# Kernel tuning notes

Hardware: AMD Instinct MI355X
Metric: run time of the kernel (lower is better)

The kernel has to match this reference:

```python
import jax, jax.numpy as jnp
import numpy as np

MARGIN = 0.3
LAMBDA_TRIPLET = 1.0
LAMBDA_ID = 1.0
EPS = 1e-6  # torch pairwise_distance eps added to the difference elementwise


def setup_inputs() -> dict:
    key = jax.random.key(0)
    k1, k2 = jax.random.split(key)
    B, N, D = 64, 512, 512
    reid_features = jax.random.normal(k1, (B, N, D), dtype=jnp.float32)
    # ids in [-1, 32): -1 marks invalid detections, as in the torch module
    track_ids = jax.random.randint(k2, (B, N), -1, 32, dtype=jnp.int32)
    return {"reid_features": reid_features, "track_ids": track_ids}


def _tracking_loss(feats, ids, margin):
    B, N, D = feats.shape
    valid = ids >= 0                                   # (B, N)
    same = ids[:, :, None] == ids[:, None, :]          # (B, N, N)
    not_self = ~jnp.eye(N, dtype=bool)                 # (N, N)
    valid_j = valid[:, None, :]                        # candidates must be valid
    pos_mask = same & not_self & valid_j               # (B, N, N)
    neg_mask = (~same) & valid_j                       # (B, N, N)
    has_pos = pos_mask.any(-1)                         # (B, N)
    has_neg = neg_mask.any(-1)
    enough = valid.sum(-1) >= 2                        # (B,)
    anchor_ok = valid & has_pos & has_neg & enough[:, None]
    # torch.nonzero(mask)[0] == first True index -> argmax on bool
    pos_idx = jnp.argmax(pos_mask, axis=-1)            # (B, N)
    neg_idx = jnp.argmax(neg_mask, axis=-1)
    p = jnp.take_along_axis(feats, pos_idx[..., None], axis=1)  # (B, N, D)
    n = jnp.take_along_axis(feats, neg_idx[..., None], axis=1)
    d_ap = jnp.sqrt(jnp.sum((feats - p + EPS) ** 2, axis=-1))   # (B, N)
    d_an = jnp.sqrt(jnp.sum((feats - n + EPS) ** 2, axis=-1))
    per_anchor = jnp.maximum(d_ap - d_an + margin, 0.0)
    num_triplets = anchor_ok.sum()
    total = jnp.sum(per_anchor * anchor_ok.astype(feats.dtype))
    loss = jnp.where(num_triplets > 0,
                     total / jnp.maximum(num_triplets, 1).astype(feats.dtype),
                     jnp.zeros((), feats.dtype))
    return loss * LAMBDA_TRIPLET


def reference(reid_features, track_ids):
    loss_triplet = _tracking_loss(reid_features, track_ids, MARGIN)
    loss_id = jnp.zeros((), reid_features.dtype)
    tracking_loss = loss_triplet + loss_id
    return tracking_loss, loss_triplet, loss_id
```

## Files before the change

### kernel.cpp

```cpp
#include <hip/hip_runtime.h>

#define MARGIN 0.3f
#define EPS 1e-6f

constexpr int B = 64, N = 512, D = 512;
constexpr int NIDS = 32;
constexpr int BLOCKS = 512;
constexpr int THREADS = 512;
constexpr int WAVES = THREADS / 64;
constexpr int ANCH_PER_BLOCK = N / 8;
constexpr int ANCH_PER_WAVE = ANCH_PER_BLOCK / WAVES;

__global__ __launch_bounds__(THREADS) void tl_main(const float* __restrict__ feats,
                                                   const int* __restrict__ ids,
                                                   float* __restrict__ psum,
                                                   float* __restrict__ pcnt) {
    __shared__ int s_ids[N];
    __shared__ int s_first[NIDS], s_second[NIDS];
    __shared__ int s_j0, s_jdiff, s_vcnt;
    __shared__ float s_wsum[WAVES];
    __shared__ int s_wcnt[WAVES];

    const int t = threadIdx.x;
    const int b = blockIdx.x >> 3;
    const int seg = (blockIdx.x & 7) * ANCH_PER_BLOCK;
    const int* __restrict__ bid = ids + b * N;

    if (t < NIDS) { s_first[t] = N; s_second[t] = N; }
    if (t == 0) { s_j0 = N; s_jdiff = N; s_vcnt = 0; }
    __syncthreads();

    {
        const int v = bid[t];
        s_ids[t] = v;
        if (v >= 0) {
            atomicMin(&s_first[v], t);
            atomicMin(&s_j0, t);
            atomicAdd(&s_vcnt, 1);
        }
    }
    __syncthreads();
    const int id0 = (s_j0 < N) ? s_ids[s_j0] : -2;
    {
        const int v = s_ids[t];
        if (v >= 0) {
            if (s_first[v] != t) atomicMin(&s_second[v], t);
            if (v != id0) atomicMin(&s_jdiff, t);
        }
    }
    __syncthreads();

    const int lane = t & 63;
    const int wave = t >> 6;
    const float* __restrict__ bf = feats + (size_t)b * N * D;
    const int vcnt = s_vcnt;
    const int j0 = s_j0, jdiff = s_jdiff;

    float wsum = 0.0f;
    int wcnt = 0;

    #pragma unroll
    for (int k = 0; k < ANCH_PER_WAVE; ++k) {
        const int i = seg + wave * ANCH_PER_WAVE + k;
        const int v = s_ids[i];
        bool ok = false;
        int posj = 0, negj = 0;
        if (v >= 0 && vcnt >= 2) {
            posj = (s_first[v] != i) ? s_first[v] : s_second[v];
            negj = (id0 != v) ? j0 : jdiff;
            ok = (posj < N) && (negj < N);
        }
        if (ok) {
            const float4* fa = (const float4*)(bf + (size_t)i * D) + lane * 2;
            const float4* fp = (const float4*)(bf + (size_t)posj * D) + lane * 2;
            const float4* fn = (const float4*)(bf + (size_t)negj * D) + lane * 2;
            float sap = 0.0f, san = 0.0f;
            #pragma unroll
            for (int q = 0; q < 2; ++q) {
                const float4 a = fa[q];
                const float4 p = fp[q];
                const float4 n = fn[q];
                float d;
                d = a.x - p.x + EPS; sap += d * d;
                d = a.y - p.y + EPS; sap += d * d;
                d = a.z - p.z + EPS; sap += d * d;
                d = a.w - p.w + EPS; sap += d * d;
                d = a.x - n.x + EPS; san += d * d;
                d = a.y - n.y + EPS; san += d * d;
                d = a.z - n.z + EPS; san += d * d;
                d = a.w - n.w + EPS; san += d * d;
            }
            #pragma unroll
            for (int off = 32; off >= 1; off >>= 1) {
                sap += __shfl_xor(sap, off);
                san += __shfl_xor(san, off);
            }
            wsum += fmaxf(sqrtf(sap) - sqrtf(san) + MARGIN, 0.0f);
            ++wcnt;
        }
    }

    if (lane == 0) { s_wsum[wave] = wsum; s_wcnt[wave] = wcnt; }
    __syncthreads();
    if (t == 0) {
        float s = 0.0f; int c = 0;
        #pragma unroll
        for (int w = 0; w < WAVES; ++w) { s += s_wsum[w]; c += s_wcnt[w]; }
        psum[blockIdx.x] = s;
        pcnt[blockIdx.x] = (float)c;
    }
}

__global__ __launch_bounds__(256) void tl_finalize(const float* __restrict__ psum,
                                                   const float* __restrict__ pcnt,
                                                   float* __restrict__ out) {
    __shared__ float s_s[4], s_c[4];
    const int t = threadIdx.x;
    float s = 0.0f, c = 0.0f;
    for (int k = t; k < BLOCKS; k += 256) { s += psum[k]; c += pcnt[k]; }
    #pragma unroll
    for (int off = 32; off >= 1; off >>= 1) {
        s += __shfl_xor(s, off);
        c += __shfl_xor(c, off);
    }
    if ((t & 63) == 0) { s_s[t >> 6] = s; s_c[t >> 6] = c; }
    __syncthreads();
    if (t == 0) {
        const float S = s_s[0] + s_s[1] + s_s[2] + s_s[3];
        const float C = s_c[0] + s_c[1] + s_c[2] + s_c[3];
        const float loss = (C > 0.0f) ? (S / C) : 0.0f;
        out[0] = loss;
        out[1] = loss;
        out[2] = 0.0f;
    }
}

extern "C" void kernel_launch(void* const* d_in, const int* in_sizes, int n_in,
                              void* d_out, int out_size, void* d_ws, size_t ws_size,
                              hipStream_t stream) {
    const float* feats = (const float*)d_in[0];
    const int* ids = (const int*)d_in[1];
    float* out = (float*)d_out;

    float* psum = (float*)d_ws;
    float* pcnt = psum + BLOCKS;

    tl_main<<<BLOCKS, THREADS, 0, stream>>>(feats, ids, psum, pcnt);
    tl_finalize<<<1, 256, 0, stream>>>(psum, pcnt, out);
}
```

Baseline: 105.0 us.

## Precompute pos/neg index tables in separate kernel and preload shared negatives

Adds a per-batch table-building kernel that writes each anchor's positive and negative indices plus the two candidate negative rows. The main kernel then uses 2048 smaller blocks of 256 threads that read this table instead of rebuilding the id tables in each block. Each wave loads the two possible negative rows once and picks between them per anchor, and anchor loads are made branch-free. The intent is to cut redundant per-block table setup and negative-row traffic and to improve occupancy. The cost is an extra kernel launch and a small global-memory round trip for the descriptor table.

```diff
diff --git a/kernel.cpp b/kernel.cpp
--- a/kernel.cpp
+++ b/kernel.cpp
@@ -5,99 +5,118 @@
 
 constexpr int B = 64, N = 512, D = 512;
 constexpr int NIDS = 32;
-constexpr int BLOCKS = 512;
-constexpr int THREADS = 512;
-constexpr int WAVES = THREADS / 64;
-constexpr int ANCH_PER_BLOCK = N / 8;
-constexpr int ANCH_PER_WAVE = ANCH_PER_BLOCK / WAVES;
 
-__global__ __launch_bounds__(THREADS) void tl_main(const float* __restrict__ feats,
-                                                   const int* __restrict__ ids,
-                                                   float* __restrict__ psum,
-                                                   float* __restrict__ pcnt) {
+constexpr int MB_THREADS = 256;
+constexpr int MB_WAVES = MB_THREADS / 64;
+constexpr int ANCH_PER_WAVE = 4;
+constexpr int MB_BLOCKS = (B * N) / (MB_WAVES * ANCH_PER_WAVE);
+
+
+__global__ __launch_bounds__(512) void tl_tables(const int* __restrict__ ids,
+                                                 int2* __restrict__ desc,
+                                                 int2* __restrict__ hdr) {
     __shared__ int s_ids[N];
     __shared__ int s_first[NIDS], s_second[NIDS];
     __shared__ int s_j0, s_jdiff, s_vcnt;
-    __shared__ float s_wsum[WAVES];
-    __shared__ int s_wcnt[WAVES];
-
     const int t = threadIdx.x;
-    const int b = blockIdx.x >> 3;
-    const int seg = (blockIdx.x & 7) * ANCH_PER_BLOCK;
-    const int* __restrict__ bid = ids + b * N;
+    const int b = blockIdx.x;
 
     if (t < NIDS) { s_first[t] = N; s_second[t] = N; }
     if (t == 0) { s_j0 = N; s_jdiff = N; s_vcnt = 0; }
     __syncthreads();
 
-    {
-        const int v = bid[t];
-        s_ids[t] = v;
-        if (v >= 0) {
-            atomicMin(&s_first[v], t);
-            atomicMin(&s_j0, t);
-            atomicAdd(&s_vcnt, 1);
-        }
+    const int v = ids[b * N + t];
+    s_ids[t] = v;
+    if (v >= 0) {
+        atomicMin(&s_first[v], t);
+        atomicMin(&s_j0, t);
+        atomicAdd(&s_vcnt, 1);
     }
     __syncthreads();
     const int id0 = (s_j0 < N) ? s_ids[s_j0] : -2;
-    {
-        const int v = s_ids[t];
-        if (v >= 0) {
-            if (s_first[v] != t) atomicMin(&s_second[v], t);
-            if (v != id0) atomicMin(&s_jdiff, t);
-        }
+    if (v >= 0) {
+        if (s_first[v] != t) atomicMin(&s_second[v], t);
+        if (v != id0) atomicMin(&s_jdiff, t);
     }
     __syncthreads();
 
+    int2 d = make_int2(-1, -1);
+    if (v >= 0 && s_vcnt >= 2) {
+        const int posj = (s_first[v] != t) ? s_first[v] : s_second[v];
+        const int negj = (v != id0) ? s_j0 : s_jdiff;
+        if (posj < N && negj < N) d = make_int2(posj, negj);
+    }
+    desc[b * N + t] = d;
+    if (t == 0) hdr[b] = make_int2(min(s_j0, N - 1), min(s_jdiff, N - 1));
+}
+
+__global__ __launch_bounds__(MB_THREADS, 4) void tl_main(const float* __restrict__ feats,
+                                                         const int2* __restrict__ desc,
+                                                         const int2* __restrict__ hdr,
+                                                         float* __restrict__ psum,
+                                                         float* __restrict__ pcnt) {
+    __shared__ float s_wsum[MB_WAVES];
+    __shared__ int s_wcnt[MB_WAVES];
+
+    const int t = threadIdx.x;
     const int lane = t & 63;
     const int wave = t >> 6;
+    const int gw = blockIdx.x * MB_WAVES + wave;
+    const int b = gw >> 7;
+    const int i0 = (gw & 127) * ANCH_PER_WAVE;
     const float* __restrict__ bf = feats + (size_t)b * N * D;
-    const int vcnt = s_vcnt;
-    const int j0 = s_j0, jdiff = s_jdiff;
+
+    const int2 h = hdr[b];
+    const float4* n0p = (const float4*)(bf + (size_t)h.x * D) + lane * 2;
+    const float4* n1p = (const float4*)(bf + (size_t)h.y * D) + lane * 2;
+    const float4 n0a = n0p[0], n0b = n0p[1];
+    const float4 n1a = n1p[0], n1b = n1p[1];
 
     float wsum = 0.0f;
     int wcnt = 0;
 
     #pragma unroll
     for (int k = 0; k < ANCH_PER_WAVE; ++k) {
-        const int i = seg + wave * ANCH_PER_WAVE + k;
-        const int v = s_ids[i];
-        bool ok = false;
-        int posj = 0, negj = 0;
-        if (v >= 0 && vcnt >= 2) {
-            posj = (s_first[v] != i) ? s_first[v] : s_second[v];
-            negj = (id0 != v) ? j0 : jdiff;
-            ok = (posj < N) && (negj < N);
+        const int i = i0 + k;
+        const int2 d = desc[b * N + i];
+        const bool ok = (d.x >= 0);
+        const int pj = ok ? d.x : 0;
+
+        const float4* fa = (const float4*)(bf + (size_t)i * D) + lane * 2;
+        const float4* fp = (const float4*)(bf + (size_t)pj * D) + lane * 2;
+        const float4 a0 = fa[0], a1 = fa[1];
+        const float4 p0 = fp[0], p1 = fp[1];
+
+        const bool useN0 = (d.y == h.x);
+        const float4 m0 = useN0 ? n0a : n1a;
+        const float4 m1 = useN0 ? n0b : n1b;
+
+        float sap = 0.0f, san = 0.0f, dd;
+        dd = a0.x - p0.x + EPS; sap += dd * dd;
+        dd = a0.y - p0.y + EPS; sap += dd * dd;
+        dd = a0.z - p0.z + EPS; sap += dd * dd;
+        dd = a0.w - p0.w + EPS; sap += dd * dd;
+        dd = a1.x - p1.x + EPS; sap += dd * dd;
+        dd = a1.y - p1.y + EPS; sap += dd * dd;
+        dd = a1.z - p1.z + EPS; sap += dd * dd;
+        dd = a1.w - p1.w + EPS; sap += dd * dd;
+        dd = a0.x - m0.x + EPS; san += dd * dd;
+        dd = a0.y - m0.y + EPS; san += dd * dd;
+        dd = a0.z - m0.z + EPS; san += dd * dd;
+        dd = a0.w - m0.w + EPS; san += dd * dd;
+        dd = a1.x - m1.x + EPS; san += dd * dd;
+        dd = a1.y - m1.y + EPS; san += dd * dd;
+        dd = a1.z - m1.z + EPS; san += dd * dd;
+        dd = a1.w - m1.w + EPS; san += dd * dd;
+
+        #pragma unroll
+        for (int off = 32; off >= 1; off >>= 1) {
+            sap += __shfl_xor(sap, off);
+            san += __shfl_xor(san, off);
         }
-        if (ok) {
-            const float4* fa = (const float4*)(bf + (size_t)i * D) + lane * 2;
-            const float4* fp = (const float4*)(bf + (size_t)posj * D) + lane * 2;
-            const float4* fn = (const float4*)(bf + (size_t)negj * D) + lane * 2;
-            float sap = 0.0f, san = 0.0f;
-            #pragma unroll
-            for (int q = 0; q < 2; ++q) {
-                const float4 a = fa[q];
-                const float4 p = fp[q];
-                const float4 n = fn[q];
-                float d;
-                d = a.x - p.x + EPS; sap += d * d;
-                d = a.y - p.y + EPS; sap += d * d;
-                d = a.z - p.z + EPS; sap += d * d;
-                d = a.w - p.w + EPS; sap += d * d;
-                d = a.x - n.x + EPS; san += d * d;
-                d = a.y - n.y + EPS; san += d * d;
-                d = a.z - n.z + EPS; san += d * d;
-                d = a.w - n.w + EPS; san += d * d;
-            }
-            #pragma unroll
-            for (int off = 32; off >= 1; off >>= 1) {
-                sap += __shfl_xor(sap, off);
-                san += __shfl_xor(san, off);
-            }
-            wsum += fmaxf(sqrtf(sap) - sqrtf(san) + MARGIN, 0.0f);
-            ++wcnt;
-        }
+        const float per = fmaxf(sqrtf(sap) - sqrtf(san) + MARGIN, 0.0f);
+        wsum += ok ? per : 0.0f;
+        wcnt += ok ? 1 : 0;
     }
 
     if (lane == 0) { s_wsum[wave] = wsum; s_wcnt[wave] = wcnt; }
@@ -105,7 +124,7 @@
     if (t == 0) {
         float s = 0.0f; int c = 0;
         #pragma unroll
-        for (int w = 0; w < WAVES; ++w) { s += s_wsum[w]; c += s_wcnt[w]; }
+        for (int w = 0; w < MB_WAVES; ++w) { s += s_wsum[w]; c += s_wcnt[w]; }
         psum[blockIdx.x] = s;
         pcnt[blockIdx.x] = (float)c;
     }
@@ -117,7 +136,7 @@
     __shared__ float s_s[4], s_c[4];
     const int t = threadIdx.x;
     float s = 0.0f, c = 0.0f;
-    for (int k = t; k < BLOCKS; k += 256) { s += psum[k]; c += pcnt[k]; }
+    for (int k = t; k < MB_BLOCKS; k += 256) { s += psum[k]; c += pcnt[k]; }
     #pragma unroll
     for (int off = 32; off >= 1; off >>= 1) {
         s += __shfl_xor(s, off);
@@ -142,9 +161,13 @@
     const int* ids = (const int*)d_in[1];
     float* out = (float*)d_out;
 
-    float* psum = (float*)d_ws;
-    float* pcnt = psum + BLOCKS;
+    char* ws = (char*)d_ws;
+    int2* desc = (int2*)ws;
+    int2* hdr = (int2*)(ws + sizeof(int2) * B * N);
+    float* psum = (float*)(ws + sizeof(int2) * (B * N + B));
+    float* pcnt = psum + MB_BLOCKS;
 
-    tl_main<<<BLOCKS, THREADS, 0, stream>>>(feats, ids, psum, pcnt);
+    tl_tables<<<B, 512, 0, stream>>>(ids, desc, hdr);
+    tl_main<<<MB_BLOCKS, MB_THREADS, 0, stream>>>(feats, desc, hdr, psum, pcnt);
     tl_finalize<<<1, 256, 0, stream>>>(psum, pcnt, out);
 }
```

Result: no change. 104.9 us (-0.1%).
